# Kernel tuning notes

Measured on AMD Instinct MI355X. Metric: run time of the kernel, lower is better.

The kernel has to match this reference:

```python
import jax, jax.numpy as jnp
import numpy as np

B, H, S, D = 4, 16, 2048, 64
NEG = -1000000000.0  # matches torch masked_fill constant


def setup_inputs() -> dict:
    key = jax.random.key(0)
    kq, kk, kv, km = jax.random.split(key, 4)
    q = jax.random.normal(kq, (B, H, S, D), dtype=jnp.float32)
    k = jax.random.normal(kk, (B, H, S, D), dtype=jnp.float32)
    v = jax.random.normal(kv, (B, H, S, D), dtype=jnp.float32)
    mask = jax.random.randint(km, (B, S), 0, 2, dtype=jnp.int32)
    return {"q": q, "k": k, "v": v, "mask": mask}


def reference(q, k, v, mask):
    # NOTE: original module applies NO 1/sqrt(d) scaling despite its name.
    # scores: [B, H, S, S]
    attn = jnp.einsum("bhqd,bhkd->bhqk", q, k)
    # mask [B, S] -> [B, 1, 1, S]; masked_fill where mask == 0
    m = mask[:, None, None, :]
    attn = jnp.where(m == 0, jnp.float32(NEG), attn)
    attn = jax.nn.softmax(attn, axis=-1)
    # dropout p=0.0 -> identity
    output = jnp.einsum("bhqk,bhkd->bhqd", attn, v)
    return (output, attn)
```

## Files before the change

### kernel.cpp

```cpp
#include <hip/hip_runtime.h>

typedef _Float16 f16x8 __attribute__((ext_vector_type(8)));
typedef float    f32x4 __attribute__((ext_vector_type(4)));

#define BHn 64
#define SEQ 2048
#define DIM 64
static const size_t ELEMS = (size_t)BHn * SEQ * DIM;

#define LDS_BARRIER() asm volatile("s_waitcnt lgkmcnt(0)\n\ts_barrier" ::: "memory")

__global__ __launch_bounds__(256) void convert_kv2(
    const float* __restrict__ k, const float* __restrict__ v,
    _Float16* __restrict__ v16, _Float16* __restrict__ k16)
{
  __shared__ _Float16 lt[64 * 68];
  const int blk = blockIdx.x;
  const int tid = threadIdx.x;

  if (blk < 2048) {
    const int bh   = blk >> 5;
    const int ch   = blk & 31;
    const int row0 = ch * 64;
    {
      const int rr = tid >> 4;
      const int c4 = (tid & 15) << 2;
#pragma unroll
      for (int i = 0; i < 4; ++i) {
        const int r = i*16 + rr;
        float4 x = *(const float4*)(v + ((size_t)(bh*SEQ + row0 + r))*DIM + c4);
        _Float16* dst = &lt[r*68 + c4];
        dst[0] = (_Float16)x.x; dst[1] = (_Float16)x.y;
        dst[2] = (_Float16)x.z; dst[3] = (_Float16)x.w;
      }
    }
    __syncthreads();
#pragma unroll
    for (int h = 0; h < 2; ++h) {
      const int gr   = tid + h*256;
      const int lane = gr & 63;
      const int wt   = (gr >> 6) & 3;
      const int ul   = gr >> 8;
      const int l15  = lane & 15, g = lane >> 4;
      const int d    = wt*16 + l15;
      const int rb   = ul*32 + g*8;
      f16x8 o;
#pragma unroll
      for (int j = 0; j < 8; ++j) o[j] = lt[(rb + j)*68 + d];
      const int u = ch*2 + ul;
      *(f16x8*)(v16 + (((size_t)((bh*64 + u)*4 + wt))*64 + lane)*8) = o;
    }
  } else {
    const int gi   = (blk - 2048)*256 + tid;
    const int c8   = gi & 7;
    const int rowg = gi >> 3;
    const int row  = rowg & 2047;
    const int bh   = rowg >> 11;
    const float* src = k + (size_t)gi * 8;
    float4 a  = *(const float4*)src;
    float4 bx = *(const float4*)(src + 4);
    f16x8 o;
    o[0]=(_Float16)a.x;  o[1]=(_Float16)a.y;  o[2]=(_Float16)a.z;  o[3]=(_Float16)a.w;
    o[4]=(_Float16)bx.x; o[5]=(_Float16)bx.y; o[6]=(_Float16)bx.z; o[7]=(_Float16)bx.w;
    const int kt = row >> 4, l15r = row & 15;
    const int s  = c8 >> 2,  g    = c8 & 3;
    *(f16x8*)(k16 + ((size_t)((bh*128 + kt)*2 + s))*512 + (g*16 + l15r)*8) = o;
  }
}

template<bool KWS>
__global__ __launch_bounds__(512, 4) void attn_fused(
    const float* __restrict__ q, const float* __restrict__ kf32,
    const int* __restrict__ mask,
    const _Float16* __restrict__ k16, const _Float16* __restrict__ v16,
    float* __restrict__ outO, float* __restrict__ outA)
{
  __shared__ _Float16 P16[16 * SEQ];
  __shared__ float    redf[128];

  const int blk  = blockIdx.x;
  const int bh   = blk >> 7;
  const int qt   = blk & 127;
  const int b    = bh >> 4;
  const int tid  = threadIdx.x;
  const int w    = tid >> 6;
  const int lane = tid & 63;
  const int l15  = lane & 15;
  const int g    = lane >> 4;

  const int* mrow = mask + (size_t)b * SEQ;
  unsigned mk = 0;
#pragma unroll
  for (int t = 0; t < 16; ++t)
    mk |= (mrow[(w << 8) + (t << 4) + l15] != 0) ? (1u << t) : 0u;

  const float* qp = q + ((size_t)(bh * SEQ + qt * 16 + l15)) * DIM + g * 8;
  f16x8 qf0, qf1;
  {
    float4 a0 = *(const float4*)(qp);
    float4 a1 = *(const float4*)(qp + 4);
    float4 b0 = *(const float4*)(qp + 32);
    float4 b1 = *(const float4*)(qp + 36);
    qf0[0]=(_Float16)a0.x; qf0[1]=(_Float16)a0.y; qf0[2]=(_Float16)a0.z; qf0[3]=(_Float16)a0.w;
    qf0[4]=(_Float16)a1.x; qf0[5]=(_Float16)a1.y; qf0[6]=(_Float16)a1.z; qf0[7]=(_Float16)a1.w;
    qf1[0]=(_Float16)b0.x; qf1[1]=(_Float16)b0.y; qf1[2]=(_Float16)b0.z; qf1[3]=(_Float16)b0.w;
    qf1[4]=(_Float16)b1.x; qf1[5]=(_Float16)b1.y; qf1[6]=(_Float16)b1.z; qf1[7]=(_Float16)b1.w;
  }

  f32x4 acc[16];
  const f32x4 zz = {0.f, 0.f, 0.f, 0.f};
#pragma unroll
  for (int t = 0; t < 16; ++t) acc[t] = zz;

  __builtin_amdgcn_s_setprio(1);
#pragma unroll
  for (int t = 0; t < 16; ++t) {
    const int kt = (w << 4) + t;
    f16x8 b0, b1;
    if constexpr (KWS) {
      const _Float16* kp = k16 + ((size_t)((bh * 128 + kt) * 2)) * 512 + lane * 8;
      b0 = *(const f16x8*)(kp);
      b1 = *(const f16x8*)(kp + 512);
    } else {
      const float* kp = kf32 + ((size_t)(bh * SEQ + kt * 16 + l15)) * DIM + g * 8;
      float4 x0 = *(const float4*)(kp);
      float4 x1 = *(const float4*)(kp + 4);
      float4 y0 = *(const float4*)(kp + 32);
      float4 y1 = *(const float4*)(kp + 36);
      b0[0]=(_Float16)x0.x; b0[1]=(_Float16)x0.y; b0[2]=(_Float16)x0.z; b0[3]=(_Float16)x0.w;
      b0[4]=(_Float16)x1.x; b0[5]=(_Float16)x1.y; b0[6]=(_Float16)x1.z; b0[7]=(_Float16)x1.w;
      b1[0]=(_Float16)y0.x; b1[1]=(_Float16)y0.y; b1[2]=(_Float16)y0.z; b1[3]=(_Float16)y0.w;
      b1[4]=(_Float16)y1.x; b1[5]=(_Float16)y1.y; b1[6]=(_Float16)y1.z; b1[7]=(_Float16)y1.w;
    }
    acc[t] = __builtin_amdgcn_mfma_f32_16x16x32_f16(qf0, b0, acc[t], 0, 0, 0);
    acc[t] = __builtin_amdgcn_mfma_f32_16x16x32_f16(qf1, b1, acc[t], 0, 0, 0);
  }
  __builtin_amdgcn_s_setprio(0);

  float s0=0.f, s1=0.f, s2=0.f, s3=0.f;
#pragma unroll
  for (int t = 0; t < 16; ++t) {
    const bool on = (mk >> t) & 1u;
    float e0 = on ? __expf(acc[t][0]) : 0.f; acc[t][0] = e0; s0 += e0;
    float e1 = on ? __expf(acc[t][1]) : 0.f; acc[t][1] = e1; s1 += e1;
    float e2 = on ? __expf(acc[t][2]) : 0.f; acc[t][2] = e2; s2 += e2;
    float e3 = on ? __expf(acc[t][3]) : 0.f; acc[t][3] = e3; s3 += e3;
  }
#pragma unroll
  for (int off = 1; off < 16; off <<= 1) {
    s0 += __shfl_xor(s0, off); s1 += __shfl_xor(s1, off);
    s2 += __shfl_xor(s2, off); s3 += __shfl_xor(s3, off);
  }
  if (l15 == 0) {
    redf[w*16 + 4*g + 0] = s0; redf[w*16 + 4*g + 1] = s1;
    redf[w*16 + 4*g + 2] = s2; redf[w*16 + 4*g + 3] = s3;
  }
  LDS_BARRIER();
  float t0, t1, t2, t3;
  {
    float4 r = *(const float4*)&redf[4*g];
    t0 = r.x; t1 = r.y; t2 = r.z; t3 = r.w;
#pragma unroll
    for (int ww = 1; ww < 8; ++ww) {
      float4 p = *(const float4*)&redf[ww*16 + 4*g];
      t0 += p.x; t1 += p.y; t2 += p.z; t3 += p.w;
    }
  }
  const float inv0 = 1.0f / t0, inv1 = 1.0f / t1, inv2 = 1.0f / t2, inv3 = 1.0f / t3;

#pragma unroll
  for (int t = 0; t < 16; ++t) {
    const int c  = (w << 8) + (t << 4) + l15;
    const int r0 = 4 * g;
    *(_Float16*)((char*)P16 + ((((r0+0)*SEQ + c)*2) ^ (((r0+0)&7)<<4))) = (_Float16)(acc[t][0] * inv0);
    *(_Float16*)((char*)P16 + ((((r0+1)*SEQ + c)*2) ^ (((r0+1)&7)<<4))) = (_Float16)(acc[t][1] * inv1);
    *(_Float16*)((char*)P16 + ((((r0+2)*SEQ + c)*2) ^ (((r0+2)&7)<<4))) = (_Float16)(acc[t][2] * inv2);
    *(_Float16*)((char*)P16 + ((((r0+3)*SEQ + c)*2) ^ (((r0+3)&7)<<4))) = (_Float16)(acc[t][3] * inv3);
  }
  LDS_BARRIER();

  f32x4 o0 = zz, o1 = zz, o2 = zz, o3 = zz;
  const size_t arowbase = (size_t)(bh * SEQ + qt * 16);
#pragma unroll
  for (int uu = 0; uu < 8; ++uu) {
    const int u = uu * 8 + w;
    const f16x8 pa = *(const f16x8*)((const char*)P16 +
                     (((l15*SEQ + u*32 + g*8)*2) ^ ((l15&7)<<4)));
    const _Float16* vp = v16 + ((size_t)((bh*64 + u)*4))*512 + lane*8;
    __builtin_amdgcn_s_setprio(1);
    o0 = __builtin_amdgcn_mfma_f32_16x16x32_f16(pa, *(const f16x8*)(vp       ), o0, 0, 0, 0);
    o1 = __builtin_amdgcn_mfma_f32_16x16x32_f16(pa, *(const f16x8*)(vp +  512), o1, 0, 0, 0);
    o2 = __builtin_amdgcn_mfma_f32_16x16x32_f16(pa, *(const f16x8*)(vp + 1024), o2, 0, 0, 0);
    o3 = __builtin_amdgcn_mfma_f32_16x16x32_f16(pa, *(const f16x8*)(vp + 1536), o3, 0, 0, 0);
    __builtin_amdgcn_s_setprio(0);
#pragma unroll
    for (int h2 = 0; h2 < 2; ++h2) {
      const int it = uu * 2 + h2;
      const int cb = tid << 2;
      union { uint2 u2; _Float16 hh[4]; } cv;
      cv.u2 = *(const uint2*)((const char*)P16 + (((it*SEQ + cb)*2) ^ ((it&7)<<4)));
      f32x4 ov;
      ov[0] = (float)cv.hh[0]; ov[1] = (float)cv.hh[1];
      ov[2] = (float)cv.hh[2]; ov[3] = (float)cv.hh[3];
      __builtin_nontemporal_store(ov, (f32x4*)(outA + (arowbase + it)*SEQ + cb));
    }
  }
  LDS_BARRIER();

  float* Opart = (float*)P16;
#pragma unroll
  for (int i = 0; i < 4; ++i) {
    Opart[(w*16 + 4*g + i)*64 +  0 + l15] = o0[i];
    Opart[(w*16 + 4*g + i)*64 + 16 + l15] = o1[i];
    Opart[(w*16 + 4*g + i)*64 + 32 + l15] = o2[i];
    Opart[(w*16 + 4*g + i)*64 + 48 + l15] = o3[i];
  }
  LDS_BARRIER();
  if (tid < 256) {
    const int r = tid >> 4;
    const int d = (tid & 15) << 2;
    f32x4 s = *(const f32x4*)&Opart[r*64 + d];
#pragma unroll
    for (int ww = 1; ww < 8; ++ww) {
      f32x4 p = *(const f32x4*)&Opart[(ww*16 + r)*64 + d];
      s += p;
    }
    __builtin_nontemporal_store(s, (f32x4*)(outO + ((size_t)(bh*SEQ + qt*16 + r))*DIM + d));
  }
}

extern "C" void kernel_launch(void* const* d_in, const int* in_sizes, int n_in,
                              void* d_out, int out_size, void* d_ws, size_t ws_size,
                              hipStream_t stream)
{
  const float* q    = (const float*)d_in[0];
  const float* k    = (const float*)d_in[1];
  const float* v    = (const float*)d_in[2];
  const int*   mask = (const int*)d_in[3];

  float* outO = (float*)d_out;
  float* outA = outO + ELEMS;

  _Float16* v16 = (_Float16*)d_ws;
  _Float16* k16 = v16 + ELEMS;
  const bool kws = (ws_size >= 2 * ELEMS * sizeof(_Float16));

  if (kws) {
    convert_kv2<<<6144, 256, 0, stream>>>(k, v, v16, k16);
    attn_fused<true ><<<8192, 512, 0, stream>>>(q, k, mask, k16, v16, outO, outA);
  } else {
    convert_kv2<<<2048, 256, 0, stream>>>(k, v, v16, k16);
    attn_fused<false><<<8192, 512, 0, stream>>>(q, k, mask, k16, v16, outO, outA);
  }
}
```

Baseline: 295.4 us.

## Process two query tiles per block, overlapping attn stores with next tile's compute

Each block now handles two consecutive 16-row query tiles with double-buffered LDS probability tiles. The first tile's attention-matrix writeback is interleaved with the second tile's QK MFMAs, and the second tile's writeback is interleaved with the first tile's PV MFMAs. Block indices are also remapped so that consecutive blocks are spread across heads. This aims to hide the large attention-output store traffic behind compute and to reuse the mask load, at the cost of doubling LDS use (occupancy drops to 2 blocks per CU) and raising register pressure.

```diff
diff --git a/kernel.cpp b/kernel.cpp
--- a/kernel.cpp
+++ b/kernel.cpp
@@ -69,24 +69,27 @@
 }
 
 template<bool KWS>
-__global__ __launch_bounds__(512, 4) void attn_fused(
+__global__ __launch_bounds__(512, 2) void attn_fused2(
     const float* __restrict__ q, const float* __restrict__ kf32,
     const int* __restrict__ mask,
     const _Float16* __restrict__ k16, const _Float16* __restrict__ v16,
     float* __restrict__ outO, float* __restrict__ outA)
 {
-  __shared__ _Float16 P16[16 * SEQ];
+  __shared__ _Float16 P16[2][16 * SEQ];
   __shared__ float    redf[128];
 
-  const int blk  = blockIdx.x;
-  const int bh   = blk >> 7;
-  const int qt   = blk & 127;
+  const int orig = blockIdx.x;
+  const int blk  = (orig & 7) * 512 + (orig >> 3);
+  const int bh   = blk >> 6;
+  const int jj   = blk & 63;
+  const int qt1  = jj * 2;
   const int b    = bh >> 4;
   const int tid  = threadIdx.x;
   const int w    = tid >> 6;
   const int lane = tid & 63;
   const int l15  = lane & 15;
   const int g    = lane >> 4;
+  const int cb   = tid << 2;
 
   const int* mrow = mask + (size_t)b * SEQ;
   unsigned mk = 0;
@@ -94,9 +97,12 @@
   for (int t = 0; t < 16; ++t)
     mk |= (mrow[(w << 8) + (t << 4) + l15] != 0) ? (1u << t) : 0u;
 
-  const float* qp = q + ((size_t)(bh * SEQ + qt * 16 + l15)) * DIM + g * 8;
+  f32x4 acc[16];
+  const f32x4 zz = {0.f, 0.f, 0.f, 0.f};
   f16x8 qf0, qf1;
-  {
+
+  {
+    const float* qp = q + ((size_t)(bh * SEQ + qt1 * 16 + l15)) * DIM + g * 8;
     float4 a0 = *(const float4*)(qp);
     float4 a1 = *(const float4*)(qp + 4);
     float4 b0 = *(const float4*)(qp + 32);
@@ -106,12 +112,8 @@
     qf1[0]=(_Float16)b0.x; qf1[1]=(_Float16)b0.y; qf1[2]=(_Float16)b0.z; qf1[3]=(_Float16)b0.w;
     qf1[4]=(_Float16)b1.x; qf1[5]=(_Float16)b1.y; qf1[6]=(_Float16)b1.z; qf1[7]=(_Float16)b1.w;
   }
-
-  f32x4 acc[16];
-  const f32x4 zz = {0.f, 0.f, 0.f, 0.f};
 #pragma unroll
   for (int t = 0; t < 16; ++t) acc[t] = zz;
-
   __builtin_amdgcn_s_setprio(1);
 #pragma unroll
   for (int t = 0; t < 16; ++t) {
@@ -123,10 +125,8 @@
       b1 = *(const f16x8*)(kp + 512);
     } else {
       const float* kp = kf32 + ((size_t)(bh * SEQ + kt * 16 + l15)) * DIM + g * 8;
-      float4 x0 = *(const float4*)(kp);
-      float4 x1 = *(const float4*)(kp + 4);
-      float4 y0 = *(const float4*)(kp + 32);
-      float4 y1 = *(const float4*)(kp + 36);
+      float4 x0 = *(const float4*)(kp);     float4 x1 = *(const float4*)(kp + 4);
+      float4 y0 = *(const float4*)(kp + 32); float4 y1 = *(const float4*)(kp + 36);
       b0[0]=(_Float16)x0.x; b0[1]=(_Float16)x0.y; b0[2]=(_Float16)x0.z; b0[3]=(_Float16)x0.w;
       b0[4]=(_Float16)x1.x; b0[5]=(_Float16)x1.y; b0[6]=(_Float16)x1.z; b0[7]=(_Float16)x1.w;
       b1[0]=(_Float16)y0.x; b1[1]=(_Float16)y0.y; b1[2]=(_Float16)y0.z; b1[3]=(_Float16)y0.w;
@@ -137,95 +137,207 @@
   }
   __builtin_amdgcn_s_setprio(0);
 
-  float s0=0.f, s1=0.f, s2=0.f, s3=0.f;
+  {
+    float s0=0.f, s1=0.f, s2=0.f, s3=0.f;
+#pragma unroll
+    for (int t = 0; t < 16; ++t) {
+      const bool on = (mk >> t) & 1u;
+      float e0 = on ? __expf(acc[t][0]) : 0.f; acc[t][0] = e0; s0 += e0;
+      float e1 = on ? __expf(acc[t][1]) : 0.f; acc[t][1] = e1; s1 += e1;
+      float e2 = on ? __expf(acc[t][2]) : 0.f; acc[t][2] = e2; s2 += e2;
+      float e3 = on ? __expf(acc[t][3]) : 0.f; acc[t][3] = e3; s3 += e3;
+    }
+#pragma unroll
+    for (int off = 1; off < 16; off <<= 1) {
+      s0 += __shfl_xor(s0, off); s1 += __shfl_xor(s1, off);
+      s2 += __shfl_xor(s2, off); s3 += __shfl_xor(s3, off);
+    }
+    if (l15 == 0) {
+      redf[w*16 + 4*g + 0] = s0; redf[w*16 + 4*g + 1] = s1;
+      redf[w*16 + 4*g + 2] = s2; redf[w*16 + 4*g + 3] = s3;
+    }
+    LDS_BARRIER();
+    float t0, t1, t2, t3;
+    {
+      float4 r = *(const float4*)&redf[4*g];
+      t0 = r.x; t1 = r.y; t2 = r.z; t3 = r.w;
+#pragma unroll
+      for (int ww = 1; ww < 8; ++ww) {
+        float4 p = *(const float4*)&redf[ww*16 + 4*g];
+        t0 += p.x; t1 += p.y; t2 += p.z; t3 += p.w;
+      }
+    }
+    const float inv0 = 1.0f/t0, inv1 = 1.0f/t1, inv2 = 1.0f/t2, inv3 = 1.0f/t3;
+#pragma unroll
+    for (int t = 0; t < 16; ++t) {
+      const int c  = (w << 8) + (t << 4) + l15;
+      const int r0 = 4 * g;
+      char* base = (char*)&P16[0][0];
+      *(_Float16*)(base + ((((r0+0)*SEQ + c)*2) ^ (((r0+0)&7)<<4))) = (_Float16)(acc[t][0] * inv0);
+      *(_Float16*)(base + ((((r0+1)*SEQ + c)*2) ^ (((r0+1)&7)<<4))) = (_Float16)(acc[t][1] * inv1);
+      *(_Float16*)(base + ((((r0+2)*SEQ + c)*2) ^ (((r0+2)&7)<<4))) = (_Float16)(acc[t][2] * inv2);
+      *(_Float16*)(base + ((((r0+3)*SEQ + c)*2) ^ (((r0+3)&7)<<4))) = (_Float16)(acc[t][3] * inv3);
+    }
+  }
+  LDS_BARRIER();
+
+  const size_t arow1 = (size_t)(bh * SEQ + qt1 * 16);
+  const size_t arow2 = arow1 + 16;
+  {
+    const float* qp = q + ((size_t)(bh * SEQ + (qt1+1) * 16 + l15)) * DIM + g * 8;
+    float4 a0 = *(const float4*)(qp);
+    float4 a1 = *(const float4*)(qp + 4);
+    float4 b0 = *(const float4*)(qp + 32);
+    float4 b1 = *(const float4*)(qp + 36);
+    qf0[0]=(_Float16)a0.x; qf0[1]=(_Float16)a0.y; qf0[2]=(_Float16)a0.z; qf0[3]=(_Float16)a0.w;
+    qf0[4]=(_Float16)a1.x; qf0[5]=(_Float16)a1.y; qf0[6]=(_Float16)a1.z; qf0[7]=(_Float16)a1.w;
+    qf1[0]=(_Float16)b0.x; qf1[1]=(_Float16)b0.y; qf1[2]=(_Float16)b0.z; qf1[3]=(_Float16)b0.w;
+    qf1[4]=(_Float16)b1.x; qf1[5]=(_Float16)b1.y; qf1[6]=(_Float16)b1.z; qf1[7]=(_Float16)b1.w;
+  }
+#pragma unroll
+  for (int t = 0; t < 16; ++t) acc[t] = zz;
 #pragma unroll
   for (int t = 0; t < 16; ++t) {
-    const bool on = (mk >> t) & 1u;
-    float e0 = on ? __expf(acc[t][0]) : 0.f; acc[t][0] = e0; s0 += e0;
-    float e1 = on ? __expf(acc[t][1]) : 0.f; acc[t][1] = e1; s1 += e1;
-    float e2 = on ? __expf(acc[t][2]) : 0.f; acc[t][2] = e2; s2 += e2;
-    float e3 = on ? __expf(acc[t][3]) : 0.f; acc[t][3] = e3; s3 += e3;
-  }
-#pragma unroll
-  for (int off = 1; off < 16; off <<= 1) {
-    s0 += __shfl_xor(s0, off); s1 += __shfl_xor(s1, off);
-    s2 += __shfl_xor(s2, off); s3 += __shfl_xor(s3, off);
-  }
-  if (l15 == 0) {
-    redf[w*16 + 4*g + 0] = s0; redf[w*16 + 4*g + 1] = s1;
-    redf[w*16 + 4*g + 2] = s2; redf[w*16 + 4*g + 3] = s3;
+    const int kt = (w << 4) + t;
+    f16x8 b0, b1;
+    if constexpr (KWS) {
+      const _Float16* kp = k16 + ((size_t)((bh * 128 + kt) * 2)) * 512 + lane * 8;
+      b0 = *(const f16x8*)(kp);
+      b1 = *(const f16x8*)(kp + 512);
+    } else {
+      const float* kp = kf32 + ((size_t)(bh * SEQ + kt * 16 + l15)) * DIM + g * 8;
+      float4 x0 = *(const float4*)(kp);     float4 x1 = *(const float4*)(kp + 4);
+      float4 y0 = *(const float4*)(kp + 32); float4 y1 = *(const float4*)(kp + 36);
+      b0[0]=(_Float16)x0.x; b0[1]=(_Float16)x0.y; b0[2]=(_Float16)x0.z; b0[3]=(_Float16)x0.w;
+      b0[4]=(_Float16)x1.x; b0[5]=(_Float16)x1.y; b0[6]=(_Float16)x1.z; b0[7]=(_Float16)x1.w;
+      b1[0]=(_Float16)y0.x; b1[1]=(_Float16)y0.y; b1[2]=(_Float16)y0.z; b1[3]=(_Float16)y0.w;
+      b1[4]=(_Float16)y1.x; b1[5]=(_Float16)y1.y; b1[6]=(_Float16)y1.z; b1[7]=(_Float16)y1.w;
+    }
+    __builtin_amdgcn_s_setprio(1);
+    acc[t] = __builtin_amdgcn_mfma_f32_16x16x32_f16(qf0, b0, acc[t], 0, 0, 0);
+    acc[t] = __builtin_amdgcn_mfma_f32_16x16x32_f16(qf1, b1, acc[t], 0, 0, 0);
+    __builtin_amdgcn_s_setprio(0);
+    {
+      union { uint2 u2; _Float16 hh[4]; } cv;
+      cv.u2 = *(const uint2*)((const char*)&P16[0][0] + (((t*SEQ + cb)*2) ^ ((t&7)<<4)));
+      f32x4 ov;
+      ov[0] = (float)cv.hh[0]; ov[1] = (float)cv.hh[1];
+      ov[2] = (float)cv.hh[2]; ov[3] = (float)cv.hh[3];
+      __builtin_nontemporal_store(ov, (f32x4*)(outA + (arow1 + t)*SEQ + cb));
+    }
+  }
+
+  {
+    float s0=0.f, s1=0.f, s2=0.f, s3=0.f;
+#pragma unroll
+    for (int t = 0; t < 16; ++t) {
+      const bool on = (mk >> t) & 1u;
+      float e0 = on ? __expf(acc[t][0]) : 0.f; acc[t][0] = e0; s0 += e0;
+      float e1 = on ? __expf(acc[t][1]) : 0.f; acc[t][1] = e1; s1 += e1;
+      float e2 = on ? __expf(acc[t][2]) : 0.f; acc[t][2] = e2; s2 += e2;
+      float e3 = on ? __expf(acc[t][3]) : 0.f; acc[t][3] = e3; s3 += e3;
+    }
+#pragma unroll
+    for (int off = 1; off < 16; off <<= 1) {
+      s0 += __shfl_xor(s0, off); s1 += __shfl_xor(s1, off);
+      s2 += __shfl_xor(s2, off); s3 += __shfl_xor(s3, off);
+    }
+    if (l15 == 0) {
+      redf[w*16 + 4*g + 0] = s0; redf[w*16 + 4*g + 1] = s1;
+      redf[w*16 + 4*g + 2] = s2; redf[w*16 + 4*g + 3] = s3;
+    }
+    LDS_BARRIER();
+    float t0, t1, t2, t3;
+    {
+      float4 r = *(const float4*)&redf[4*g];
+      t0 = r.x; t1 = r.y; t2 = r.z; t3 = r.w;
+#pragma unroll
+      for (int ww = 1; ww < 8; ++ww) {
+        float4 p = *(const float4*)&redf[ww*16 + 4*g];
+        t0 += p.x; t1 += p.y; t2 += p.z; t3 += p.w;
+      }
+    }
+    const float inv0 = 1.0f/t0, inv1 = 1.0f/t1, inv2 = 1.0f/t2, inv3 = 1.0f/t3;
+#pragma unroll
+    for (int t = 0; t < 16; ++t) {
+      const int c  = (w << 8) + (t << 4) + l15;
+      const int r0 = 4 * g;
+      char* base = (char*)&P16[1][0];
+      *(_Float16*)(base + ((((r0+0)*SEQ + c)*2) ^ (((r0+0)&7)<<4))) = (_Float16)(acc[t][0] * inv0);
+      *(_Float16*)(base + ((((r0+1)*SEQ + c)*2) ^ (((r0+1)&7)<<4))) = (_Float16)(acc[t][1] * inv1);
+      *(_Float16*)(base + ((((r0+2)*SEQ + c)*2) ^ (((r0+2)&7)<<4))) = (_Float16)(acc[t][2] * inv2);
+      *(_Float16*)(base + ((((r0+3)*SEQ + c)*2) ^ (((r0+3)&7)<<4))) = (_Float16)(acc[t][3] * inv3);
+    }
   }
   LDS_BARRIER();
-  float t0, t1, t2, t3;
-  {
-    float4 r = *(const float4*)&redf[4*g];
-    t0 = r.x; t1 = r.y; t2 = r.z; t3 = r.w;
-#pragma unroll
-    for (int ww = 1; ww < 8; ++ww) {
-      float4 p = *(const float4*)&redf[ww*16 + 4*g];
-      t0 += p.x; t1 += p.y; t2 += p.z; t3 += p.w;
-    }
-  }
-  const float inv0 = 1.0f / t0, inv1 = 1.0f / t1, inv2 = 1.0f / t2, inv3 = 1.0f / t3;
-
-#pragma unroll
-  for (int t = 0; t < 16; ++t) {
-    const int c  = (w << 8) + (t << 4) + l15;
-    const int r0 = 4 * g;
-    *(_Float16*)((char*)P16 + ((((r0+0)*SEQ + c)*2) ^ (((r0+0)&7)<<4))) = (_Float16)(acc[t][0] * inv0);
-    *(_Float16*)((char*)P16 + ((((r0+1)*SEQ + c)*2) ^ (((r0+1)&7)<<4))) = (_Float16)(acc[t][1] * inv1);
-    *(_Float16*)((char*)P16 + ((((r0+2)*SEQ + c)*2) ^ (((r0+2)&7)<<4))) = (_Float16)(acc[t][2] * inv2);
-    *(_Float16*)((char*)P16 + ((((r0+3)*SEQ + c)*2) ^ (((r0+3)&7)<<4))) = (_Float16)(acc[t][3] * inv3);
-  }
-  LDS_BARRIER();
-
-  f32x4 o0 = zz, o1 = zz, o2 = zz, o3 = zz;
-  const size_t arowbase = (size_t)(bh * SEQ + qt * 16);
+
+  f32x4 o10 = zz, o11 = zz, o12 = zz, o13 = zz;
+  f32x4 o20 = zz, o21 = zz, o22 = zz, o23 = zz;
 #pragma unroll
   for (int uu = 0; uu < 8; ++uu) {
     const int u = uu * 8 + w;
-    const f16x8 pa = *(const f16x8*)((const char*)P16 +
+    const f16x8 pa = *(const f16x8*)((const char*)&P16[0][0] +
                      (((l15*SEQ + u*32 + g*8)*2) ^ ((l15&7)<<4)));
     const _Float16* vp = v16 + ((size_t)((bh*64 + u)*4))*512 + lane*8;
     __builtin_amdgcn_s_setprio(1);
-    o0 = __builtin_amdgcn_mfma_f32_16x16x32_f16(pa, *(const f16x8*)(vp       ), o0, 0, 0, 0);
-    o1 = __builtin_amdgcn_mfma_f32_16x16x32_f16(pa, *(const f16x8*)(vp +  512), o1, 0, 0, 0);
-    o2 = __builtin_amdgcn_mfma_f32_16x16x32_f16(pa, *(const f16x8*)(vp + 1024), o2, 0, 0, 0);
-    o3 = __builtin_amdgcn_mfma_f32_16x16x32_f16(pa, *(const f16x8*)(vp + 1536), o3, 0, 0, 0);
+    o10 = __builtin_amdgcn_mfma_f32_16x16x32_f16(pa, *(const f16x8*)(vp       ), o10, 0, 0, 0);
+    o11 = __builtin_amdgcn_mfma_f32_16x16x32_f16(pa, *(const f16x8*)(vp +  512), o11, 0, 0, 0);
+    o12 = __builtin_amdgcn_mfma_f32_16x16x32_f16(pa, *(const f16x8*)(vp + 1024), o12, 0, 0, 0);
+    o13 = __builtin_amdgcn_mfma_f32_16x16x32_f16(pa, *(const f16x8*)(vp + 1536), o13, 0, 0, 0);
     __builtin_amdgcn_s_setprio(0);
 #pragma unroll
     for (int h2 = 0; h2 < 2; ++h2) {
       const int it = uu * 2 + h2;
-      const int cb = tid << 2;
       union { uint2 u2; _Float16 hh[4]; } cv;
-      cv.u2 = *(const uint2*)((const char*)P16 + (((it*SEQ + cb)*2) ^ ((it&7)<<4)));
+      cv.u2 = *(const uint2*)((const char*)&P16[1][0] + (((it*SEQ + cb)*2) ^ ((it&7)<<4)));
       f32x4 ov;
       ov[0] = (float)cv.hh[0]; ov[1] = (float)cv.hh[1];
       ov[2] = (float)cv.hh[2]; ov[3] = (float)cv.hh[3];
-      __builtin_nontemporal_store(ov, (f32x4*)(outA + (arowbase + it)*SEQ + cb));
-    }
+      __builtin_nontemporal_store(ov, (f32x4*)(outA + (arow2 + it)*SEQ + cb));
+    }
+  }
+#pragma unroll
+  for (int uu = 0; uu < 8; ++uu) {
+    const int u = uu * 8 + w;
+    const f16x8 pa = *(const f16x8*)((const char*)&P16[1][0] +
+                     (((l15*SEQ + u*32 + g*8)*2) ^ ((l15&7)<<4)));
+    const _Float16* vp = v16 + ((size_t)((bh*64 + u)*4))*512 + lane*8;
+    __builtin_amdgcn_s_setprio(1);
+    o20 = __builtin_amdgcn_mfma_f32_16x16x32_f16(pa, *(const f16x8*)(vp       ), o20, 0, 0, 0);
+    o21 = __builtin_amdgcn_mfma_f32_16x16x32_f16(pa, *(const f16x8*)(vp +  512), o21, 0, 0, 0);
+    o22 = __builtin_amdgcn_mfma_f32_16x16x32_f16(pa, *(const f16x8*)(vp + 1024), o22, 0, 0, 0);
+    o23 = __builtin_amdgcn_mfma_f32_16x16x32_f16(pa, *(const f16x8*)(vp + 1536), o23, 0, 0, 0);
+    __builtin_amdgcn_s_setprio(0);
   }
   LDS_BARRIER();
 
-  float* Opart = (float*)P16;
+  float* Opart = (float*)&P16[0][0];
 #pragma unroll
   for (int i = 0; i < 4; ++i) {
-    Opart[(w*16 + 4*g + i)*64 +  0 + l15] = o0[i];
-    Opart[(w*16 + 4*g + i)*64 + 16 + l15] = o1[i];
-    Opart[(w*16 + 4*g + i)*64 + 32 + l15] = o2[i];
-    Opart[(w*16 + 4*g + i)*64 + 48 + l15] = o3[i];
+    const int rowb = (w*16 + 4*g + i)*64;
+    Opart[rowb +  0 + l15] = o10[i];
+    Opart[rowb + 16 + l15] = o11[i];
+    Opart[rowb + 32 + l15] = o12[i];
+    Opart[rowb + 48 + l15] = o13[i];
+    Opart[8192 + rowb +  0 + l15] = o20[i];
+    Opart[8192 + rowb + 16 + l15] = o21[i];
+    Opart[8192 + rowb + 32 + l15] = o22[i];
+    Opart[8192 + rowb + 48 + l15] = o23[i];
   }
   LDS_BARRIER();
-  if (tid < 256) {
-    const int r = tid >> 4;
-    const int d = (tid & 15) << 2;
-    f32x4 s = *(const f32x4*)&Opart[r*64 + d];
+  {
+    const int tile = tid >> 8;
+    const int r    = (tid & 255) >> 4;
+    const int d    = (tid & 15) << 2;
+    const float* Op = Opart + tile * 8192;
+    f32x4 s = *(const f32x4*)&Op[r*64 + d];
 #pragma unroll
     for (int ww = 1; ww < 8; ++ww) {
-      f32x4 p = *(const f32x4*)&Opart[(ww*16 + r)*64 + d];
+      f32x4 p = *(const f32x4*)&Op[(ww*16 + r)*64 + d];
       s += p;
     }
-    __builtin_nontemporal_store(s, (f32x4*)(outO + ((size_t)(bh*SEQ + qt*16 + r))*DIM + d));
+    __builtin_nontemporal_store(s,
+        (f32x4*)(outO + ((size_t)(bh*SEQ + (qt1+tile)*16 + r))*DIM + d));
   }
 }
 
@@ -247,9 +359,9 @@
 
   if (kws) {
     convert_kv2<<<6144, 256, 0, stream>>>(k, v, v16, k16);
-    attn_fused<true ><<<8192, 512, 0, stream>>>(q, k, mask, k16, v16, outO, outA);
+    attn_fused2<true ><<<4096, 512, 0, stream>>>(q, k, mask, k16, v16, outO, outA);
   } else {
     convert_kv2<<<2048, 256, 0, stream>>>(k, v, v16, k16);
-    attn_fused<false><<<8192, 512, 0, stream>>>(q, k, mask, k16, v16, outO, outA);
+    attn_fused2<false><<<4096, 512, 0, stream>>>(q, k, mask, k16, v16, outO, outA);
   }
 }
```

Result: slower. 347.7 us (+17.7%).
